# Performance work log

Measured on AMD Instinct MI355X. Metric: run time of the kernel, lower is better.

## Reference

```python
import jax, jax.numpy as jnp
import numpy as np

BOHR_RADIUS = 0.529177  # Angstrom
KE_KCAL = 332.0636      # Coulomb constant, kcal/mol * Angstrom / e^2
EPS = 1e-15
R_CUT = 5.0

ZBL = {'d': [0.8854 * BOHR_RADIUS], 'z_exp': [0.23],
       'c': [0.1818, 0.5099, 0.2802, 0.02817],
       'exponents': [3.2, 0.9423, 0.4028, 0.2016]}

def _inv_softplus(v):
    v = np.asarray(v, dtype=np.float32)
    return jnp.asarray(np.log(np.exp(v) - 1.0).reshape(-1, 1))

def setup_inputs() -> dict:
    key = jax.random.key(0)
    k1, k2, k3, k4 = jax.random.split(key, 4)
    N, E, M = 200000, 8000000, 1000
    xyz = jax.random.normal(k1, (N, 3), dtype=jnp.float32) * 3.0
    z = jax.random.randint(k2, (N,), 1, 94, dtype=jnp.int32)
    nbrs = jax.random.randint(k3, (E, 2), 0, N, dtype=jnp.int32)
    offsets = jax.random.normal(k4, (E, 3), dtype=jnp.float32) * 2.0
    num_atoms = jnp.full((M,), N // M, dtype=jnp.int32)
    return {
        'xyz': xyz, 'z': z, 'nbrs': nbrs, 'num_atoms': num_atoms, 'offsets': offsets,
        'd_inv': _inv_softplus(ZBL['d']),
        'z_exp_inv': _inv_softplus(ZBL['z_exp']),
        'c_inv': _inv_softplus(ZBL['c']),
        'exponents_inv': _inv_softplus(ZBL['exponents']),
    }

def reference(xyz, z, nbrs, num_atoms, offsets, d_inv, z_exp_inv, c_inv, exponents_inv):
    sp = jax.nn.softplus
    d, z_exp, c, exponents = sp(d_inv), sp(z_exp_inv), sp(c_inv), sp(exponents_inv)

    i, j = nbrs[:, 0], nbrs[:, 1]
    mask = j > i  # undirected-edge filter (masked instead of gathered: same math)

    z_i = z[i].astype(jnp.float32)  # [E]
    z_j = z[j].astype(jnp.float32)
    diff = xyz[i] - xyz[j] - offsets                  # [E,3]
    r_ij = jnp.sqrt((diff ** 2 + EPS).sum(-1))        # stable norm, [E]

    # ZBL phi: d,z_exp are [1,1]; broadcast over edges
    a = (d / (z_i ** z_exp + z_j ** z_exp)).reshape(-1)           # [E]
    phi = (c * jnp.exp(-exponents * r_ij / a)).sum(0) / c.sum()   # [4,E] -> [E]

    # SpookyNet cutoff, NaN-safe outside r_cut
    den = (R_CUT - r_ij) * (R_CUT + r_ij)
    safe_den = jnp.where(r_ij < R_CUT, den, 1.0)
    f_cut = jnp.where(r_ij < R_CUT, jnp.exp(-r_ij ** 2 / safe_den), 0.0)

    pairwise = KE_KCAL * z_i * z_j / r_ij * phi * f_cut
    pairwise = jnp.where(mask, pairwise, 0.0)

    N = xyz.shape[0]
    M = num_atoms.shape[0]
    mol_idx = jnp.repeat(jnp.arange(M), num_atoms, total_repeat_length=N)  # [N]
    seg = mol_idx[i]                                                       # [E]
    energy = jax.ops.segment_sum(pairwise, seg, num_segments=M).reshape(-1, 1)
    return energy
```

## Files before the change

### kernel.cpp

```cpp
#include <hip/hip_runtime.h>
#include <hip/hip_bf16.h>

#define KE_F   332.0636f
#define MAX_M  1024
#define BLK    256
#define NBLK   2048
#define WCHUNK 256

typedef int   ivec2 __attribute__((ext_vector_type(2)));
typedef int   ivec4 __attribute__((ext_vector_type(4)));
typedef float fvec4 __attribute__((ext_vector_type(4)));

__device__ __forceinline__ float softplusf(float x) {
    return logf(1.0f + expf(x));
}

__device__ __forceinline__ void wave_fence() {
    __builtin_amdgcn_wave_barrier();
    asm volatile("" ::: "memory");
}

__global__ void scan_params_kernel(const int* __restrict__ num_atoms, int M,
                                   const float* __restrict__ d_inv,
                                   const float* __restrict__ z_exp_inv,
                                   const float* __restrict__ c_inv,
                                   const float* __restrict__ exp_inv,
                                   int* __restrict__ mol_starts,
                                   float* __restrict__ params,
                                   float* __restrict__ out) {
    __shared__ int buf[MAX_M];
    int t = threadIdx.x;
    buf[t] = (t < M) ? num_atoms[t] : 0;
    __syncthreads();
    for (int off = 1; off < MAX_M; off <<= 1) {
        int x = (t >= off) ? buf[t - off] : 0;
        __syncthreads();
        buf[t] += x;
        __syncthreads();
    }
    if (t == 0) mol_starts[0] = 0;
    if (t < M) mol_starts[t + 1] = buf[t];
    if (t == 0) {
        float dd = softplusf(d_inv[0]);
        float c0 = softplusf(c_inv[0]), c1 = softplusf(c_inv[1]);
        float c2 = softplusf(c_inv[2]), c3 = softplusf(c_inv[3]);
        float e0 = softplusf(exp_inv[0]), e1 = softplusf(exp_inv[1]);
        float e2 = softplusf(exp_inv[2]), e3 = softplusf(exp_inv[3]);
        float ic = 1.0f / (c0 + c1 + c2 + c3);
        float id = 1.0f / dd;
        params[0] = c0 * ic; params[1] = c1 * ic; params[2] = c2 * ic; params[3] = c3 * ic;
        params[4] = e0 * id; params[5] = e1 * id; params[6] = e2 * id; params[7] = e3 * id;
    }
    if (t < 96) {
        float zexp = softplusf(z_exp_inv[0]);
        params[16 + t] = __powf((float)t, zexp);
    }
    for (int k = t; k < M; k += MAX_M) out[k] = 0.0f;
}

__global__ void pack_kernel(const float* __restrict__ xyz,
                            const int* __restrict__ z,
                            const int* __restrict__ mol_starts, int M, int N,
                            float4* __restrict__ pack) {
    int a = blockIdx.x * blockDim.x + threadIdx.x;
    if (a >= N) return;
    int lo = 0, hi = M;
    while (hi - lo > 1) {
        int mid = (lo + hi) >> 1;
        if (mol_starts[mid] <= a) lo = mid; else hi = mid;
    }
    pack[a] = make_float4(xyz[3 * a + 0], xyz[3 * a + 1], xyz[3 * a + 2],
                          (float)((lo << 7) | z[a]));
}

__global__ __launch_bounds__(BLK) void nr_main_kernel(
    const int* __restrict__ nbrs, const float* __restrict__ offsets,
    const float4* __restrict__ pack,
    const float* __restrict__ params, float* __restrict__ out, int E, int M) {
    __shared__ float sm[MAX_M];
    __shared__ float zp[96];
    __shared__ float sof[4][WCHUNK * 3];
    for (int t = threadIdx.x; t < MAX_M; t += BLK) sm[t] = 0.0f;
    if (threadIdx.x < 96) zp[threadIdx.x] = params[16 + threadIdx.x];
    __syncthreads();

    const float4 kk = *(const float4*)(params + 0);
    const float4 gg = *(const float4*)(params + 4);

    const int lane = threadIdx.x & 63;
    float* myof = sof[threadIdx.x >> 6];

    const int nchunks = E / WCHUNK;
    const int gw = (blockIdx.x * BLK + threadIdx.x) >> 6;
    const int nw = (gridDim.x * BLK) >> 6;

    const ivec2* nbp = (const ivec2*)nbrs;
    const fvec4* of4 = (const fvec4*)offsets;

    for (int c = gw; c < nchunks; c += nw) {
        const size_t eb = (size_t)c * WCHUNK;
        ivec2 nb[4];
#pragma unroll
        for (int h = 0; h < 4; ++h)
            nb[h] = __builtin_nontemporal_load(nbp + eb + 64 * h + lane);
        const fvec4* ofb = of4 + (size_t)c * ((WCHUNK * 3) / 4);
        const fvec4 F0 = __builtin_nontemporal_load(ofb + lane);
        const fvec4 F1 = __builtin_nontemporal_load(ofb + 64 + lane);
        const fvec4 F2 = __builtin_nontemporal_load(ofb + 128 + lane);

        bool   m[4];
        float4 pi[4], pj[4];
#pragma unroll
        for (int h = 0; h < 4; ++h) {
            const int iv = nb[h].x, jv = nb[h].y;
            m[h] = jv > iv;
            pi[h] = pack[m[h] ? iv : 0];
            pj[h] = pack[m[h] ? jv : 0];
        }

        wave_fence();
        *(fvec4*)&myof[4 * lane]       = F0;
        *(fvec4*)&myof[4 * lane + 256] = F1;
        *(fvec4*)&myof[4 * lane + 512] = F2;
        wave_fence();

#pragma unroll
        for (int h = 0; h < 4; ++h) {
            const float oxv = myof[192 * h + 3 * lane + 0];
            const float oyv = myof[192 * h + 3 * lane + 1];
            const float ozv = myof[192 * h + 3 * lane + 2];
            const float dx = pi[h].x - pj[h].x - oxv;
            const float dy = pi[h].y - pj[h].y - oyv;
            const float dz = pi[h].z - pj[h].z - ozv;
            const float r2 = fmaf(dx, dx, fmaf(dy, dy, dz * dz)) + 3e-15f;
            const bool ok = m[h] && (r2 < 25.0f);
            const int  wi = (int)pi[h].w;
            const int  wj = (int)pj[h].w;
            const float zi = (float)(wi & 127);
            const float zj = (float)(wj & 127);
            const float inv_r = rsqrtf(r2);
            const float r = r2 * inv_r;
            const float S = zp[wi & 127] + zp[wj & 127];
            const float rs = r * S;
            const float phi = kk.x * __expf(-gg.x * rs) + kk.y * __expf(-gg.y * rs) +
                              kk.z * __expf(-gg.z * rs) + kk.w * __expf(-gg.w * rs);
            const float fc = __expf(-__fdividef(r2, 25.0f - r2));
            const float val = KE_F * zi * zj * inv_r * phi * fc;
            if (ok) atomicAdd(&sm[wi >> 7], val);
        }
    }

    const int stride = gridDim.x * BLK;
    for (int e = nchunks * WCHUNK + blockIdx.x * BLK + threadIdx.x; e < E; e += stride) {
        const int i = nbrs[2 * e], j = nbrs[2 * e + 1];
        if (j <= i) continue;
        const float oxs = offsets[3 * e], oys = offsets[3 * e + 1], ozs = offsets[3 * e + 2];
        const float4 pis = pack[i], pjs = pack[j];
        const float dx = pis.x - pjs.x - oxs;
        const float dy = pis.y - pjs.y - oys;
        const float dz = pis.z - pjs.z - ozs;
        const float r2 = fmaf(dx, dx, fmaf(dy, dy, dz * dz)) + 3e-15f;
        if (r2 >= 25.0f) continue;
        const int  wi = (int)pis.w;
        const int  wj = (int)pjs.w;
        const float inv_r = rsqrtf(r2);
        const float r = r2 * inv_r;
        const float S = zp[wi & 127] + zp[wj & 127];
        const float rs = r * S;
        const float phi = kk.x * __expf(-gg.x * rs) + kk.y * __expf(-gg.y * rs) +
                          kk.z * __expf(-gg.z * rs) + kk.w * __expf(-gg.w * rs);
        const float fc = __expf(-__fdividef(r2, 25.0f - r2));
        atomicAdd(&sm[wi >> 7],
                  KE_F * (float)(wi & 127) * (float)(wj & 127) * inv_r * phi * fc);
    }

    __syncthreads();
    for (int t = threadIdx.x; t < M; t += BLK) {
        const float v = sm[t];
        if (v != 0.0f) atomicAdd(&out[t], v);
    }
}

extern "C" void kernel_launch(void* const* d_in, const int* in_sizes, int n_in,
                              void* d_out, int out_size, void* d_ws, size_t ws_size,
                              hipStream_t stream) {
    const float* xyz       = (const float*)d_in[0];
    const int*   z         = (const int*)d_in[1];
    const int*   nbrs      = (const int*)d_in[2];
    const int*   num_atoms = (const int*)d_in[3];
    const float* offsets   = (const float*)d_in[4];
    const float* d_inv     = (const float*)d_in[5];
    const float* z_exp_inv = (const float*)d_in[6];
    const float* c_inv     = (const float*)d_in[7];
    const float* exp_inv   = (const float*)d_in[8];
    float* out = (float*)d_out;

    const int N = in_sizes[0] / 3;
    const int E = in_sizes[2] / 2;
    const int M = in_sizes[3];

    char* w = (char*)d_ws;
    int*    mol_starts = (int*)w;
    float*  params     = (float*)(w + 4096);
    float4* pack       = (float4*)(w + 8192);

    scan_params_kernel<<<1, MAX_M, 0, stream>>>(num_atoms, M, d_inv, z_exp_inv,
                                                c_inv, exp_inv, mol_starts,
                                                params, out);
    pack_kernel<<<(N + BLK - 1) / BLK, BLK, 0, stream>>>(xyz, z, mol_starts, M, N,
                                                         pack);
    nr_main_kernel<<<NBLK, BLK, 0, stream>>>(nbrs, offsets, pack,
                                             params, out, E, M);
}
```

Before: 240.9 us.

## Software-pipeline edge and gather loads across chunks with inline-asm global loads

Restructures the main edge loop into a two-stage software pipeline. The neighbour and offset loads for chunk c+2 and the position gathers for chunk c+1 are issued with inline-asm global_load instructions before the current chunk is computed, and explicit s_waitcnt vmcnt counts control when results are consumed. The aim is to hide the latency of the dependent gather (indices, then pack lookup) behind arithmetic and other loads. In exchange it uses more registers, drops the nontemporal load hints, relies on in-order vmcnt accounting and sched barriers, and reloads a clamped duplicate chunk at the tail.

Result: slower. 257.5 us (+6.9%).

```diff
diff --git a/kernel.cpp b/kernel.cpp
--- a/kernel.cpp
+++ b/kernel.cpp
@@ -8,7 +8,6 @@
 #define WCHUNK 256
 
 typedef int   ivec2 __attribute__((ext_vector_type(2)));
-typedef int   ivec4 __attribute__((ext_vector_type(4)));
 typedef float fvec4 __attribute__((ext_vector_type(4)));
 
 __device__ __forceinline__ float softplusf(float x) {
@@ -19,6 +18,16 @@
     __builtin_amdgcn_wave_barrier();
     asm volatile("" ::: "memory");
 }
+
+#define GLOAD2(dst, base, voff)                                     \
+    asm volatile("global_load_dwordx2 %0, %1, %2"                   \
+                 : "=v"(dst) : "v"(voff), "s"(base) : "memory")
+#define GLOAD4(dst, base, voff)                                     \
+    asm volatile("global_load_dwordx4 %0, %1, %2"                   \
+                 : "=v"(dst) : "v"(voff), "s"(base) : "memory")
+#define WAITV(n) do {                                               \
+    asm volatile("s_waitcnt vmcnt(" #n ")" ::: "memory");           \
+    __builtin_amdgcn_sched_barrier(0); } while (0)
 
 __global__ void scan_params_kernel(const int* __restrict__ num_atoms, int M,
                                    const float* __restrict__ d_inv,
@@ -94,61 +103,118 @@
     const int gw = (blockIdx.x * BLK + threadIdx.x) >> 6;
     const int nw = (gridDim.x * BLK) >> 6;
 
-    const ivec2* nbp = (const ivec2*)nbrs;
-    const fvec4* of4 = (const fvec4*)offsets;
-
-    for (int c = gw; c < nchunks; c += nw) {
-        const size_t eb = (size_t)c * WCHUNK;
-        ivec2 nb[4];
+#define ISSUE_S(ch) do {                                                      \
+        const uint32_t _nbo = (uint32_t)(ch) * (WCHUNK * 8u)  + (uint32_t)lane * 8u;  \
+        GLOAD2(nb0, nbrs, _nbo);                                              \
+        GLOAD2(nb1, nbrs, _nbo + 512u);                                       \
+        GLOAD2(nb2, nbrs, _nbo + 1024u);                                      \
+        GLOAD2(nb3, nbrs, _nbo + 1536u);                                      \
+        const uint32_t _ofo = (uint32_t)(ch) * (WCHUNK * 12u) + (uint32_t)lane * 16u; \
+        GLOAD4(F0, offsets, _ofo);                                            \
+        GLOAD4(F1, offsets, _ofo + 1024u);                                    \
+        GLOAD4(F2, offsets, _ofo + 2048u);                                    \
+    } while (0)
+
+#define MKADDR(mm, vv) do {                                                   \
+        mm[0] = nb0.y > nb0.x; mm[1] = nb1.y > nb1.x;                         \
+        mm[2] = nb2.y > nb2.x; mm[3] = nb3.y > nb3.x;                         \
+        vv[0] = (uint32_t)(mm[0] ? nb0.x : 0) * 16u;                          \
+        vv[1] = (uint32_t)(mm[0] ? nb0.y : 0) * 16u;                          \
+        vv[2] = (uint32_t)(mm[1] ? nb1.x : 0) * 16u;                          \
+        vv[3] = (uint32_t)(mm[1] ? nb1.y : 0) * 16u;                          \
+        vv[4] = (uint32_t)(mm[2] ? nb2.x : 0) * 16u;                          \
+        vv[5] = (uint32_t)(mm[2] ? nb2.y : 0) * 16u;                          \
+        vv[6] = (uint32_t)(mm[3] ? nb3.x : 0) * 16u;                          \
+        vv[7] = (uint32_t)(mm[3] ? nb3.y : 0) * 16u;                          \
+    } while (0)
+
+#define ISSUE_G(vv) do {                                                      \
+        GLOAD4(gi0, pack, vv[0]); GLOAD4(gj0, pack, vv[1]);                   \
+        GLOAD4(gi1, pack, vv[2]); GLOAD4(gj1, pack, vv[3]);                   \
+        GLOAD4(gi2, pack, vv[4]); GLOAD4(gj2, pack, vv[5]);                   \
+        GLOAD4(gi3, pack, vv[6]); GLOAD4(gj3, pack, vv[7]);                   \
+    } while (0)
+
+#define DSWRITE_F() do {                                                      \
+        *(fvec4*)&myof[4 * lane]       = F0;                                  \
+        *(fvec4*)&myof[4 * lane + 256] = F1;                                  \
+        *(fvec4*)&myof[4 * lane + 512] = F2;                                  \
+    } while (0)
+
+#define EDGE(h, GI, GJ) do {                                                  \
+        const float dx = GI.x - GJ.x - o[3 * h + 0];                          \
+        const float dy = GI.y - GJ.y - o[3 * h + 1];                          \
+        const float dz = GI.z - GJ.z - o[3 * h + 2];                          \
+        const float r2 = fmaf(dx, dx, fmaf(dy, dy, dz * dz)) + 3e-15f;        \
+        const bool ok = m[h] && (r2 < 25.0f);                                 \
+        const int  wi = (int)GI.w;                                            \
+        const int  wj = (int)GJ.w;                                            \
+        const float zi = (float)(wi & 127);                                   \
+        const float zj = (float)(wj & 127);                                   \
+        const float inv_r = rsqrtf(r2);                                       \
+        const float r = r2 * inv_r;                                           \
+        const float S = zp[wi & 127] + zp[wj & 127];                          \
+        const float rs = r * S;                                               \
+        const float phi = kk.x * __expf(-gg.x * rs) + kk.y * __expf(-gg.y * rs) + \
+                          kk.z * __expf(-gg.z * rs) + kk.w * __expf(-gg.w * rs);  \
+        const float fc = __expf(-__fdividef(r2, 25.0f - r2));                 \
+        const float val = KE_F * zi * zj * inv_r * phi * fc;                  \
+        if (ok) atomicAdd(&sm[wi >> 7], val);                                 \
+    } while (0)
+
+    int c = gw;
+    if (c < nchunks) {
+        ivec2 nb0, nb1, nb2, nb3;
+        fvec4 F0, F1, F2;
+        fvec4 gi0, gj0, gi1, gj1, gi2, gj2, gi3, gj3;
+        bool  m[4];
+
+        ISSUE_S(c);
+        WAITV(0);
+        wave_fence();
+        DSWRITE_F();
+        wave_fence();
+        uint32_t vo[8];
+        MKADDR(m, vo);
+        int nx = c + nw; if (nx >= nchunks) nx = nchunks - 1;
+        ISSUE_S(nx);
+        ISSUE_G(vo);
+
+        for (;;) {
+            WAITV(8);
+            wave_fence();
+            float o[12];
 #pragma unroll
-        for (int h = 0; h < 4; ++h)
-            nb[h] = __builtin_nontemporal_load(nbp + eb + 64 * h + lane);
-        const fvec4* ofb = of4 + (size_t)c * ((WCHUNK * 3) / 4);
-        const fvec4 F0 = __builtin_nontemporal_load(ofb + lane);
-        const fvec4 F1 = __builtin_nontemporal_load(ofb + 64 + lane);
-        const fvec4 F2 = __builtin_nontemporal_load(ofb + 128 + lane);
-
-        bool   m[4];
-        float4 pi[4], pj[4];
-#pragma unroll
-        for (int h = 0; h < 4; ++h) {
-            const int iv = nb[h].x, jv = nb[h].y;
-            m[h] = jv > iv;
-            pi[h] = pack[m[h] ? iv : 0];
-            pj[h] = pack[m[h] ? jv : 0];
+            for (int h = 0; h < 4; ++h) {
+                o[3 * h + 0] = myof[192 * h + 3 * lane + 0];
+                o[3 * h + 1] = myof[192 * h + 3 * lane + 1];
+                o[3 * h + 2] = myof[192 * h + 3 * lane + 2];
+            }
+            wave_fence();
+            DSWRITE_F();
+            wave_fence();
+            bool mn[4]; uint32_t von[8];
+            MKADDR(mn, von);
+            int nx2 = c + 2 * nw; if (nx2 >= nchunks) nx2 = nchunks - 1;
+            ISSUE_S(nx2);
+            WAITV(7);
+            EDGE(0, gi0, gj0);
+            EDGE(1, gi1, gj1);
+            EDGE(2, gi2, gj2);
+            EDGE(3, gi3, gj3);
+            ISSUE_G(von);
+            m[0] = mn[0]; m[1] = mn[1]; m[2] = mn[2]; m[3] = mn[3];
+            c += nw;
+            if (c >= nchunks) break;
         }
-
-        wave_fence();
-        *(fvec4*)&myof[4 * lane]       = F0;
-        *(fvec4*)&myof[4 * lane + 256] = F1;
-        *(fvec4*)&myof[4 * lane + 512] = F2;
-        wave_fence();
-
-#pragma unroll
-        for (int h = 0; h < 4; ++h) {
-            const float oxv = myof[192 * h + 3 * lane + 0];
-            const float oyv = myof[192 * h + 3 * lane + 1];
-            const float ozv = myof[192 * h + 3 * lane + 2];
-            const float dx = pi[h].x - pj[h].x - oxv;
-            const float dy = pi[h].y - pj[h].y - oyv;
-            const float dz = pi[h].z - pj[h].z - ozv;
-            const float r2 = fmaf(dx, dx, fmaf(dy, dy, dz * dz)) + 3e-15f;
-            const bool ok = m[h] && (r2 < 25.0f);
-            const int  wi = (int)pi[h].w;
-            const int  wj = (int)pj[h].w;
-            const float zi = (float)(wi & 127);
-            const float zj = (float)(wj & 127);
-            const float inv_r = rsqrtf(r2);
-            const float r = r2 * inv_r;
-            const float S = zp[wi & 127] + zp[wj & 127];
-            const float rs = r * S;
-            const float phi = kk.x * __expf(-gg.x * rs) + kk.y * __expf(-gg.y * rs) +
-                              kk.z * __expf(-gg.z * rs) + kk.w * __expf(-gg.w * rs);
-            const float fc = __expf(-__fdividef(r2, 25.0f - r2));
-            const float val = KE_F * zi * zj * inv_r * phi * fc;
-            if (ok) atomicAdd(&sm[wi >> 7], val);
-        }
-    }
+        WAITV(0);
+    }
+
+#undef ISSUE_S
+#undef MKADDR
+#undef ISSUE_G
+#undef DSWRITE_F
+#undef EDGE
 
     const int stride = gridDim.x * BLK;
     for (int e = nchunks * WCHUNK + blockIdx.x * BLK + threadIdx.x; e < E; e += stride) {
```
